# Performance work log

Measured on AMD Instinct MI355X. Metric: run time of the kernel, lower is better.

## Reference

```python
import jax, jax.numpy as jnp
import numpy as np

B, D_IN, D_H, D_OUT = 1024, 1024, 4096, 1024
SPARSITY = 0.5  # fraction of weights KEPT (top-k)


def setup_inputs() -> dict:
    key = jax.random.key(0)
    ks = jax.random.split(key, 13)
    def kaiming(k, shape):
        fan_in = shape[-1] if len(shape) > 1 else shape[0]
        bound = 1.0 / np.sqrt(fan_in)
        return jax.random.uniform(k, shape, jnp.float32, -bound, bound)
    inp = {
        "x":   jax.random.normal(ks[0], (B, D_IN), jnp.float32),
        "W1":  kaiming(ks[1], (D_H, D_IN)),
        "b1":  kaiming(ks[2], (D_H,)),
        "W2":  kaiming(ks[3], (D_H, D_H)),
        "b2":  kaiming(ks[4], (D_H,)),
        "W3":  kaiming(ks[5], (D_OUT, D_H)),
        "b3":  kaiming(ks[6], (D_OUT,)),
        # scores: kaiming-uniform for weights, N(0, 0.01) for biases (as in Mask.__init__)
        "sW1": kaiming(ks[7], (D_H, D_IN)),
        "sb1": 0.01 * jax.random.normal(ks[8], (D_H,), jnp.float32),
        "sW2": kaiming(ks[9], (D_H, D_H)),
        "sb2": 0.01 * jax.random.normal(ks[10], (D_H,), jnp.float32),
        "sW3": kaiming(ks[11], (D_OUT, D_H)),
        "sb3": 0.01 * jax.random.normal(ks[12], (D_OUT,), jnp.float32),
    }
    return inp


def _global_masks(scores):
    """Single fused global top-k threshold mask (replaces O(P) redundant sorts).
    Bottom (1-SPARSITY) fraction (by value rank) -> 0, top SPARSITY fraction -> 1."""
    flat = jnp.concatenate([s.ravel() for s in scores])
    n = flat.shape[0]
    j = int((1.0 - SPARSITY) * n)  # number of zeroed entries
    idx = jnp.argsort(flat)
    bin_mask = jnp.zeros((n,), flat.dtype).at[idx[j:]].set(1.0)
    # straight-through: d(mask)/d(score) = 1 (GetSubnet_global.backward returns g)
    st_mask = bin_mask + flat - jax.lax.stop_gradient(flat)
    sizes = [int(np.prod(s.shape)) for s in scores]
    offs = np.concatenate([[0], np.cumsum(sizes)])
    return [st_mask[offs[i]:offs[i + 1]].reshape(scores[i].shape)
            for i in range(len(scores))]


def reference(x, W1, b1, W2, b2, W3, b3, sW1, sb1, sW2, sb2, sW3, sb3):
    masks = _global_masks([sW1, sb1, sW2, sb2, sW3, sb3])
    mW1, mb1, mW2, mb2, mW3, mb3 = masks
    # masked params, then MLP forward (torch Linear: y = x @ W.T + b)
    h = jax.nn.relu(x @ (W1 * mW1).T + b1 * mb1)
    h = jax.nn.relu(h @ (W2 * mW2).T + b2 * mb2)
    return h @ (W3 * mW3).T + b3 * mb3
```

## Files before the change

kernel.cpp:

```cpp
#include <hip/hip_runtime.h>
#include <hip/hip_bf16.h>
#include <stdint.h>


typedef __bf16 bf16_t;
typedef __bf16 bf16x4 __attribute__((ext_vector_type(4)));
typedef __bf16 bf16x8 __attribute__((ext_vector_type(8)));
typedef float  f32x4  __attribute__((ext_vector_type(4)));

#define O1 4194304L
#define O2 4198400L
#define O3 20975616L
#define O4 20979712L
#define O5 25174016L
#define N_TOT 25175040L
#define J_RANK 12587520u
#define CAND_CAP 4096

#define WS_HIST 0u
#define WS_RES  32768u
#define WS_CNT  32784u
#define WS_CAND 32800u
#define WS_W1B  131072u
#define WS_B1F  8519680u
#define WS_W2B  8536064u
#define WS_B2F  42090496u
#define WS_W3B  42106880u
#define WS_B3F  50495488u
#define WS_H1F  50511872u
#define WS_H2F  58900480u
#define WS_FAST_END 67289088ull
#define WS_H1   131072u
#define WS_H2   8519680u

#define SWZ(row, chunk) ((((chunk) + ((row) >> 1)) & 3))

__device__ __forceinline__ unsigned int mono32(float f) {
    unsigned int u = __float_as_uint(f);
    return (u & 0x80000000u) ? ~u : (u | 0x80000000u);
}

__global__ __launch_bounds__(256) void zero_kernel(unsigned int* p, int n) {
    int i = blockIdx.x * 256 + threadIdx.x;
    if (i < n) p[i] = 0u;
}

__device__ __forceinline__ void seg_lookup(long e,
    const float* s0, const float* s1, const float* s2,
    const float* s3, const float* s4, const float* s5,
    const float** sp, long* off) {
    if (e < O1)      { *sp = s0; *off = e; }
    else if (e < O2) { *sp = s1; *off = e - O1; }
    else if (e < O3) { *sp = s2; *off = e - O2; }
    else if (e < O4) { *sp = s3; *off = e - O3; }
    else if (e < O5) { *sp = s4; *off = e - O4; }
    else             { *sp = s5; *off = e - O5; }
}

__global__ __launch_bounds__(256) void hist_kernel(
    const float* s0, const float* s1, const float* s2,
    const float* s3, const float* s4, const float* s5,
    unsigned int* hist) {
    __shared__ unsigned int lh[8192];
    for (int i = threadIdx.x; i < 8192; i += 256) lh[i] = 0u;
    __syncthreads();
    const long ng = N_TOT / 4;
    for (long g = (long)blockIdx.x * 256 + threadIdx.x; g < ng;
         g += (long)gridDim.x * 256) {
        long e = g * 4;
        const float* sp; long o;
        seg_lookup(e, s0, s1, s2, s3, s4, s5, &sp, &o);
        float4 v = *(const float4*)(sp + o);
        atomicAdd(&lh[mono32(v.x) >> 19], 1u);
        atomicAdd(&lh[mono32(v.y) >> 19], 1u);
        atomicAdd(&lh[mono32(v.z) >> 19], 1u);
        atomicAdd(&lh[mono32(v.w) >> 19], 1u);
    }
    __syncthreads();
    for (int i = threadIdx.x; i < 8192; i += 256) {
        unsigned int c = lh[i];
        if (c) atomicAdd(&hist[i], c);
    }
}

__global__ __launch_bounds__(256) void select_kernel(const unsigned int* hist,
                                                     unsigned int* res) {
    __shared__ unsigned int part[256];
    int tid = threadIdx.x;
    unsigned int s = 0;
    for (int b = tid * 32; b < tid * 32 + 32; ++b) s += hist[b];
    part[tid] = s;
    __syncthreads();
    if (tid == 0) {
        unsigned int acc = 0;
        for (int i = 0; i < 256; ++i) { unsigned int v = part[i]; part[i] = acc; acc += v; }
    }
    __syncthreads();
    unsigned int acc = part[tid];
    for (int b = tid * 32; b < tid * 32 + 32; ++b) {
        unsigned int h = hist[b];
        if (acc <= J_RANK && J_RANK < acc + h) {
            res[0] = (unsigned int)b;
            res[1] = acc;
            res[2] = J_RANK - acc;
        }
        acc += h;
    }
}

__global__ __launch_bounds__(256) void mask_apply_fast(
    const float* s0, const float* s1, const float* s2,
    const float* s3, const float* s4, const float* s5,
    const float* w0, const float* w1, const float* w2,
    const float* w3, const float* w4, const float* w5,
    bf16_t* W1b, float* b1f, bf16_t* W2b, float* b2f, bf16_t* W3b, float* b3f,
    const unsigned int* res, unsigned int* cand_cnt, unsigned long long* cand) {
    const unsigned int C = res[0];
    const long ng = N_TOT / 4;
    for (long g = (long)blockIdx.x * 256 + threadIdx.x; g < ng;
         g += (long)gridDim.x * 256) {
        long e = g * 4;
        const float* sp; long o;
        seg_lookup(e, s0, s1, s2, s3, s4, s5, &sp, &o);
        const float* wp;
        if (e < O1)      wp = w0;
        else if (e < O2) wp = w1;
        else if (e < O3) wp = w2;
        else if (e < O4) wp = w3;
        else if (e < O5) wp = w4;
        else             wp = w5;
        float4 sv = *(const float4*)(sp + o);
        float4 wv = *(const float4*)(wp + o);
#define PROC(comp, ci)                                                         \
        { unsigned int key = mono32(sv.comp); unsigned int kb = key >> 19;     \
          if (kb < C) wv.comp = 0.f;                                           \
          else if (kb == C) {                                                  \
              unsigned int slot = atomicAdd(cand_cnt, 1u);                     \
              if (slot < CAND_CAP)                                             \
                  cand[slot] = (((unsigned long long)key) << 32) |             \
                               (unsigned long long)(unsigned int)(e + ci);     \
          } }
        PROC(x, 0) PROC(y, 1) PROC(z, 2) PROC(w, 3)
#undef PROC
        if (e < O1) {
            bf16x4 b; b[0]=(__bf16)wv.x; b[1]=(__bf16)wv.y; b[2]=(__bf16)wv.z; b[3]=(__bf16)wv.w;
            *(bf16x4*)(W1b + o) = b;
        } else if (e < O2) {
            *(float4*)(b1f + o) = wv;
        } else if (e < O3) {
            bf16x4 b; b[0]=(__bf16)wv.x; b[1]=(__bf16)wv.y; b[2]=(__bf16)wv.z; b[3]=(__bf16)wv.w;
            *(bf16x4*)(W2b + o) = b;
        } else if (e < O4) {
            *(float4*)(b2f + o) = wv;
        } else if (e < O5) {
            bf16x4 b; b[0]=(__bf16)wv.x; b[1]=(__bf16)wv.y; b[2]=(__bf16)wv.z; b[3]=(__bf16)wv.w;
            *(bf16x4*)(W3b + o) = b;
        } else {
            *(float4*)(b3f + o) = wv;
        }
    }
}

__global__ __launch_bounds__(256) void finalize_fast(
    const unsigned int* res, const unsigned int* cand_cnt,
    const unsigned long long* cand,
    bf16_t* W1b, float* b1f, bf16_t* W2b, float* b2f, bf16_t* W3b, float* b3f) {
    __shared__ unsigned long long buf[CAND_CAP];
    int tid = threadIdx.x;
    unsigned int cnt = *cand_cnt; if (cnt > CAND_CAP) cnt = CAND_CAP;
    unsigned int need = res[2];   if (need > cnt) need = cnt;
    for (int i = tid; i < (int)cnt; i += 256) buf[i] = cand[i];
    __syncthreads();
    for (int i = tid; i < (int)cnt; i += 256) {
        unsigned long long me = buf[i];
        unsigned int rank = 0;
        for (unsigned int j = 0; j < cnt; ++j) rank += (buf[j] < me);
        if (rank < need) {
            long idx = (long)(unsigned int)(me & 0xFFFFFFFFu);
            if (idx < O1)      W1b[idx] = (__bf16)0.f;
            else if (idx < O2) b1f[idx - O1] = 0.f;
            else if (idx < O3) W2b[idx - O2] = (__bf16)0.f;
            else if (idx < O4) b2f[idx - O3] = 0.f;
            else if (idx < O5) W3b[idx - O4] = (__bf16)0.f;
            else               b3f[idx - O5] = 0.f;
        }
    }
}

__global__ __launch_bounds__(256) void mask_apply_kernel(
    const float* s0, const float* s1, const float* s2,
    const float* s3, const float* s4, const float* s5,
    float* w0, float* w1, float* w2, float* w3, float* w4, float* w5,
    const unsigned int* res, unsigned int* cand_cnt, unsigned long long* cand) {
    const unsigned int C = res[0];
    const long ng = N_TOT / 4;
    for (long g = (long)blockIdx.x * 256 + threadIdx.x; g < ng;
         g += (long)gridDim.x * 256) {
        long e = g * 4;
        const float* sp; long o;
        seg_lookup(e, s0, s1, s2, s3, s4, s5, &sp, &o);
        float* wp;
        if (e < O1)      wp = w0;
        else if (e < O2) wp = w1;
        else if (e < O3) wp = w2;
        else if (e < O4) wp = w3;
        else if (e < O5) wp = w4;
        else             wp = w5;
        float4 sv = *(const float4*)(sp + o);
        float4 wv = *(float4*)(wp + o);
#define PROC(comp, ci)                                                         \
        { unsigned int key = mono32(sv.comp); unsigned int kb = key >> 19;     \
          if (kb < C) wv.comp = 0.f;                                           \
          else if (kb == C) {                                                  \
              unsigned int slot = atomicAdd(cand_cnt, 1u);                     \
              if (slot < CAND_CAP)                                             \
                  cand[slot] = (((unsigned long long)key) << 32) |             \
                               (unsigned long long)(unsigned int)(e + ci);     \
          } }
        PROC(x, 0) PROC(y, 1) PROC(z, 2) PROC(w, 3)
#undef PROC
        *(float4*)(wp + o) = wv;
    }
}

__global__ __launch_bounds__(256) void finalize_kernel(
    const unsigned int* res, const unsigned int* cand_cnt,
    const unsigned long long* cand,
    float* w0, float* w1, float* w2, float* w3, float* w4, float* w5) {
    __shared__ unsigned long long buf[CAND_CAP];
    int tid = threadIdx.x;
    unsigned int cnt = *cand_cnt; if (cnt > CAND_CAP) cnt = CAND_CAP;
    unsigned int need = res[2];   if (need > cnt) need = cnt;
    for (int i = tid; i < (int)cnt; i += 256) buf[i] = cand[i];
    __syncthreads();
    for (int i = tid; i < (int)cnt; i += 256) {
        unsigned long long me = buf[i];
        unsigned int rank = 0;
        for (unsigned int j = 0; j < cnt; ++j) rank += (buf[j] < me);
        if (rank < need) {
            long idx = (long)(unsigned int)(me & 0xFFFFFFFFu);
            if (idx < O1)      w0[idx] = 0.f;
            else if (idx < O2) w1[idx - O1] = 0.f;
            else if (idx < O3) w2[idx - O2] = 0.f;
            else if (idx < O4) w3[idx - O3] = 0.f;
            else if (idx < O5) w4[idx - O4] = 0.f;
            else               w5[idx - O5] = 0.f;
        }
    }
}

__device__ __forceinline__ bf16x8 load8(const float* p) {
    float4 a = *(const float4*)p;
    float4 b = *(const float4*)(p + 4);
    bf16x8 r;
    r[0] = (__bf16)a.x; r[1] = (__bf16)a.y; r[2] = (__bf16)a.z; r[3] = (__bf16)a.w;
    r[4] = (__bf16)b.x; r[5] = (__bf16)b.y; r[6] = (__bf16)b.z; r[7] = (__bf16)b.w;
    return r;
}
__device__ __forceinline__ bf16x8 load8(const bf16_t* p) {
    return *(const bf16x8*)p;
}

template <int BM, int BN, bool RELU, typename TA, typename TB, typename TC>
__global__ __launch_bounds__(256) void gemm_bt(
    const TA* __restrict__ A, const TB* __restrict__ B,
    const float* __restrict__ bias, TC* __restrict__ C,
    int M, int N, int K) {
    constexpr int BK = 32;
    constexpr int WM = BM / 2, WN = BN / 2;
    constexpr int TM = WM / 16, TN = WN / 16;
    constexpr int CA = (BM * BK) / 8;
    constexpr int CB = (BN * BK) / 8;
    __shared__ __align__(16) bf16_t As[BM * BK];
    __shared__ __align__(16) bf16_t Bs[BN * BK];

    const int tid = threadIdx.x;
    const int w = tid >> 6, lane = tid & 63;
    const int quad = lane >> 4, l16 = lane & 15;
    const int wm = (w >> 1) * WM, wn = (w & 1) * WN;
    const int rowBase = blockIdx.y * BM;
    const int colBase = blockIdx.x * BN;

    f32x4 acc[TM][TN] = {};

    const TA* Ab = A + (size_t)rowBase * K;
    const TB* Bb = B + (size_t)colBase * K;

    for (int k0 = 0; k0 < K; k0 += BK) {
        __syncthreads();
#pragma unroll
        for (int c0 = 0; c0 < CA; c0 += 256) {
            int c = c0 + tid;
            int row = c >> 2, kc = c & 3;
            *(bf16x8*)&As[row * BK + SWZ(row, kc) * 8] =
                load8(Ab + (size_t)row * K + k0 + kc * 8);
        }
#pragma unroll
        for (int c0 = 0; c0 < CB; c0 += 256) {
            int c = c0 + tid;
            int row = c >> 2, kc = c & 3;
            *(bf16x8*)&Bs[row * BK + SWZ(row, kc) * 8] =
                load8(Bb + (size_t)row * K + k0 + kc * 8);
        }
        __syncthreads();
        bf16x8 af[TM], bfr[TN];
#pragma unroll
        for (int i = 0; i < TM; ++i) {
            int r = wm + i * 16 + l16;
            af[i] = *(const bf16x8*)&As[r * BK + SWZ(r, quad) * 8];
        }
#pragma unroll
        for (int j = 0; j < TN; ++j) {
            int r = wn + j * 16 + l16;
            bfr[j] = *(const bf16x8*)&Bs[r * BK + SWZ(r, quad) * 8];
        }
#pragma unroll
        for (int i = 0; i < TM; ++i)
#pragma unroll
            for (int j = 0; j < TN; ++j)
                acc[i][j] = __builtin_amdgcn_mfma_f32_16x16x32_bf16(
                    af[i], bfr[j], acc[i][j], 0, 0, 0);
    }

#pragma unroll
    for (int i = 0; i < TM; ++i) {
#pragma unroll
        for (int j = 0; j < TN; ++j) {
            int col = colBase + wn + j * 16 + l16;
            float bv = bias[col];
#pragma unroll
            for (int r = 0; r < 4; ++r) {
                int rowg = rowBase + wm + i * 16 + quad * 4 + r;
                float v = acc[i][j][r] + bv;
                if (RELU) v = v > 0.f ? v : 0.f;
                if constexpr (sizeof(TC) == 4)
                    C[(size_t)rowg * N + col] = v;
                else
                    C[(size_t)rowg * N + col] = (bf16_t)v;
            }
        }
    }
}

extern "C" void kernel_launch(void* const* d_in, const int* in_sizes, int n_in,
                              void* d_out, int out_size, void* d_ws, size_t ws_size,
                              hipStream_t stream) {
    const float* x  = (const float*)d_in[0];
    float* W1 = (float*)d_in[1];
    float* b1 = (float*)d_in[2];
    float* W2 = (float*)d_in[3];
    float* b2 = (float*)d_in[4];
    float* W3 = (float*)d_in[5];
    float* b3 = (float*)d_in[6];
    const float* s0 = (const float*)d_in[7];
    const float* s1 = (const float*)d_in[8];
    const float* s2 = (const float*)d_in[9];
    const float* s3 = (const float*)d_in[10];
    const float* s4 = (const float*)d_in[11];
    const float* s5 = (const float*)d_in[12];

    uint8_t* ws = (uint8_t*)d_ws;
    unsigned int* hist = (unsigned int*)(ws + WS_HIST);
    unsigned int* res  = (unsigned int*)(ws + WS_RES);
    unsigned int* cnt  = (unsigned int*)(ws + WS_CNT);
    unsigned long long* cand = (unsigned long long*)(ws + WS_CAND);
    float* OUT = (float*)d_out;

    zero_kernel<<<33, 256, 0, stream>>>((unsigned int*)ws, 8200);
    hist_kernel<<<2048, 256, 0, stream>>>(s0, s1, s2, s3, s4, s5, hist);
    select_kernel<<<1, 256, 0, stream>>>(hist, res);

    if (ws_size >= WS_FAST_END) {
        bf16_t* W1b = (bf16_t*)(ws + WS_W1B);
        float*  b1f = (float*)(ws + WS_B1F);
        bf16_t* W2b = (bf16_t*)(ws + WS_W2B);
        float*  b2f = (float*)(ws + WS_B2F);
        bf16_t* W3b = (bf16_t*)(ws + WS_W3B);
        float*  b3f = (float*)(ws + WS_B3F);
        bf16_t* H1  = (bf16_t*)(ws + WS_H1F);
        bf16_t* H2  = (bf16_t*)(ws + WS_H2F);
        mask_apply_fast<<<2048, 256, 0, stream>>>(
            s0, s1, s2, s3, s4, s5, x ? (const float*)d_in[1] : W1, b1, W2, b2, W3, b3,
            W1b, b1f, W2b, b2f, W3b, b3f, res, cnt, cand);
        finalize_fast<<<1, 256, 0, stream>>>(res, cnt, cand,
                                             W1b, b1f, W2b, b2f, W3b, b3f);
        gemm_bt<64, 128, true, float, bf16_t, bf16_t>
            <<<dim3(32, 16), 256, 0, stream>>>(x, W1b, b1f, H1, 1024, 4096, 1024);
        gemm_bt<64, 128, true, bf16_t, bf16_t, bf16_t>
            <<<dim3(32, 16), 256, 0, stream>>>(H1, W2b, b2f, H2, 1024, 4096, 4096);
        gemm_bt<64, 64, false, bf16_t, bf16_t, float>
            <<<dim3(16, 16), 256, 0, stream>>>(H2, W3b, b3f, OUT, 1024, 1024, 4096);
    } else {
        bf16_t* H1 = (bf16_t*)(ws + WS_H1);
        bf16_t* H2 = (bf16_t*)(ws + WS_H2);
        mask_apply_kernel<<<2048, 256, 0, stream>>>(s0, s1, s2, s3, s4, s5,
                                                    W1, b1, W2, b2, W3, b3,
                                                    res, cnt, cand);
        finalize_kernel<<<1, 256, 0, stream>>>(res, cnt, cand,
                                               W1, b1, W2, b2, W3, b3);
        gemm_bt<64, 128, true, float, float, bf16_t>
            <<<dim3(32, 16), 256, 0, stream>>>(x, W1, b1, H1, 1024, 4096, 1024);
        gemm_bt<64, 128, true, bf16_t, float, bf16_t>
            <<<dim3(32, 16), 256, 0, stream>>>(H1, W2, b2, H2, 1024, 4096, 4096);
        gemm_bt<64, 64, false, bf16_t, float, float>
            <<<dim3(16, 16), 256, 0, stream>>>(H2, W3, b3, OUT, 1024, 1024, 4096);
    }
}
```

Baseline: 428.6 us.

## Add direct global-to-LDS bf16 GEMM with split-K for final layer

Introduces a new GEMM kernel that loads bf16 operand tiles straight into LDS with global_load_lds and a rotated swizzle, skipping the register round-trip. The last layer switches to a 64x128 tile with 4-way split-K and atomic float adds, which needs a pre-zeroed output, so a zero kernel is added. The histogram grid is also halved. Atomic accumulation makes the output order nondeterministic and adds a zeroing pass.

New measurement: 410.7 us. 1.04x faster.

```diff
diff --git a/kernel.cpp b/kernel.cpp
--- a/kernel.cpp
+++ b/kernel.cpp
@@ -7,6 +7,9 @@
 typedef __bf16 bf16x4 __attribute__((ext_vector_type(4)));
 typedef __bf16 bf16x8 __attribute__((ext_vector_type(8)));
 typedef float  f32x4  __attribute__((ext_vector_type(4)));
+
+using gvoid = const __attribute__((address_space(1))) void;
+using svoid = __attribute__((address_space(3))) void;
 
 #define O1 4194304L
 #define O2 4198400L
@@ -342,6 +345,109 @@
     }
 }
 
+template <int BM, int BN, bool RELU, int SPLITK, typename TA, typename TC>
+__global__ __launch_bounds__(256) void gemm_fast(
+    const TA* __restrict__ A, const bf16_t* __restrict__ B,
+    const float* __restrict__ bias, TC* __restrict__ C,
+    int M, int N, int K) {
+    constexpr int BK = 32;
+    constexpr int WM = BM / 2, WN = BN / 2;
+    constexpr int TM = WM / 16, TN = WN / 16;
+    constexpr int CA = (BM * BK) / 8;
+    constexpr int CB = (BN * BK) / 8;
+    __shared__ __align__(16) bf16_t As[BM * BK];
+    __shared__ __align__(16) bf16_t Bs[BN * BK];
+
+    const int tid = threadIdx.x;
+    const int w = tid >> 6, lane = tid & 63;
+    const int quad = lane >> 4, l16 = lane & 15;
+    const int wm = (w >> 1) * WM, wn = (w & 1) * WN;
+    const int rowBase = blockIdx.y * BM;
+    const int colBase = blockIdx.x * BN;
+
+    f32x4 acc[TM][TN] = {};
+
+    const TA* Ab = A + (size_t)rowBase * K;
+    const bf16_t* Bb = B + (size_t)colBase * K;
+
+    const int kPart = K / SPLITK;
+    const int kBeg = (SPLITK > 1) ? (int)blockIdx.z * kPart : 0;
+
+    for (int k0 = kBeg; k0 < kBeg + kPart; k0 += BK) {
+        if constexpr (sizeof(TA) == 2) {
+#pragma unroll
+            for (int c0 = 0; c0 < CA; c0 += 256) {
+                int c = c0 + tid;
+                int row = c >> 2, phys = c & 3;
+                int lc = (phys - (row >> 1)) & 3;
+                __builtin_amdgcn_global_load_lds(
+                    (gvoid*)(Ab + (size_t)row * K + k0 + lc * 8),
+                    (svoid*)(As + c * 8), 16, 0, 0);
+            }
+        } else {
+#pragma unroll
+            for (int c0 = 0; c0 < CA; c0 += 256) {
+                int c = c0 + tid;
+                int row = c >> 2, kc = c & 3;
+                *(bf16x8*)&As[row * BK + SWZ(row, kc) * 8] =
+                    load8(Ab + (size_t)row * K + k0 + kc * 8);
+            }
+        }
+#pragma unroll
+        for (int c0 = 0; c0 < CB; c0 += 256) {
+            int c = c0 + tid;
+            int row = c >> 2, phys = c & 3;
+            int lc = (phys - (row >> 1)) & 3;
+            __builtin_amdgcn_global_load_lds(
+                (gvoid*)(Bb + (size_t)row * K + k0 + lc * 8),
+                (svoid*)(Bs + c * 8), 16, 0, 0);
+        }
+        __syncthreads();
+
+        bf16x8 af[TM], bfr[TN];
+#pragma unroll
+        for (int i = 0; i < TM; ++i) {
+            int r = wm + i * 16 + l16;
+            af[i] = *(const bf16x8*)&As[r * BK + SWZ(r, quad) * 8];
+        }
+#pragma unroll
+        for (int j = 0; j < TN; ++j) {
+            int r = wn + j * 16 + l16;
+            bfr[j] = *(const bf16x8*)&Bs[r * BK + SWZ(r, quad) * 8];
+        }
+#pragma unroll
+        for (int i = 0; i < TM; ++i)
+#pragma unroll
+            for (int j = 0; j < TN; ++j)
+                acc[i][j] = __builtin_amdgcn_mfma_f32_16x16x32_bf16(
+                    af[i], bfr[j], acc[i][j], 0, 0, 0);
+        __syncthreads();
+    }
+
+#pragma unroll
+    for (int i = 0; i < TM; ++i) {
+#pragma unroll
+        for (int j = 0; j < TN; ++j) {
+            int col = colBase + wn + j * 16 + l16;
+            float bv = (SPLITK == 1 || blockIdx.z == 0) ? bias[col] : 0.f;
+#pragma unroll
+            for (int r = 0; r < 4; ++r) {
+                int rowg = rowBase + wm + i * 16 + quad * 4 + r;
+                float v = acc[i][j][r] + bv;
+                if constexpr (SPLITK == 1) {
+                    if (RELU) v = v > 0.f ? v : 0.f;
+                    if constexpr (sizeof(TC) == 4)
+                        C[(size_t)rowg * N + col] = v;
+                    else
+                        C[(size_t)rowg * N + col] = (bf16_t)v;
+                } else {
+                    atomicAdd((float*)&C[(size_t)rowg * N + col], v);
+                }
+            }
+        }
+    }
+}
+
 extern "C" void kernel_launch(void* const* d_in, const int* in_sizes, int n_in,
                               void* d_out, int out_size, void* d_ws, size_t ws_size,
                               hipStream_t stream) {
@@ -367,7 +473,7 @@
     float* OUT = (float*)d_out;
 
     zero_kernel<<<33, 256, 0, stream>>>((unsigned int*)ws, 8200);
-    hist_kernel<<<2048, 256, 0, stream>>>(s0, s1, s2, s3, s4, s5, hist);
+    hist_kernel<<<1024, 256, 0, stream>>>(s0, s1, s2, s3, s4, s5, hist);
     select_kernel<<<1, 256, 0, stream>>>(hist, res);
 
     if (ws_size >= WS_FAST_END) {
@@ -379,17 +485,18 @@
         float*  b3f = (float*)(ws + WS_B3F);
         bf16_t* H1  = (bf16_t*)(ws + WS_H1F);
         bf16_t* H2  = (bf16_t*)(ws + WS_H2F);
+        zero_kernel<<<4096, 256, 0, stream>>>((unsigned int*)OUT, 1048576);
         mask_apply_fast<<<2048, 256, 0, stream>>>(
-            s0, s1, s2, s3, s4, s5, x ? (const float*)d_in[1] : W1, b1, W2, b2, W3, b3,
+            s0, s1, s2, s3, s4, s5, W1, b1, W2, b2, W3, b3,
             W1b, b1f, W2b, b2f, W3b, b3f, res, cnt, cand);
         finalize_fast<<<1, 256, 0, stream>>>(res, cnt, cand,
                                              W1b, b1f, W2b, b2f, W3b, b3f);
-        gemm_bt<64, 128, true, float, bf16_t, bf16_t>
+        gemm_fast<64, 128, true, 1, float, bf16_t>
             <<<dim3(32, 16), 256, 0, stream>>>(x, W1b, b1f, H1, 1024, 4096, 1024);
-        gemm_bt<64, 128, true, bf16_t, bf16_t, bf16_t>
+        gemm_fast<64, 128, true, 1, bf16_t, bf16_t>
             <<<dim3(32, 16), 256, 0, stream>>>(H1, W2b, b2f, H2, 1024, 4096, 4096);
-        gemm_bt<64, 64, false, bf16_t, bf16_t, float>
-            <<<dim3(16, 16), 256, 0, stream>>>(H2, W3b, b3f, OUT, 1024, 1024, 4096);
+        gemm_fast<64, 128, false, 4, bf16_t, float>
+            <<<dim3(8, 16, 4), 256, 0, stream>>>(H2, W3b, b3f, OUT, 1024, 1024, 4096);
     } else {
         bf16_t* H1 = (bf16_t*)(ws + WS_H1);
         bf16_t* H2 = (bf16_t*)(ws + WS_H2);
```
